# Optimization experiments

Hardware: AMD Instinct MI355X
Metric: run time of the kernel (lower is better)

Reference implementation:

```python
import jax, jax.numpy as jnp
import numpy as np

SEQ_LEN = 512
DIM = 256
HEADS = 8
DIM_HEAD = 32
INNER = HEADS * DIM_HEAD
BATCH = 1
LN_EPS = 1e-5


def setup_inputs() -> dict:
    key = jax.random.key(0)
    ks = jax.random.split(key, 6)
    # kaiming_uniform_(a=sqrt(5)) on [L, in, out] -> bound = 1/sqrt(fan_in) with fan_in = in_dim*out_dim? 
    # torch computes fan_in from dims [1:] => fan_in = in_dim (dim of -2) * ... in practice bound ~ sqrt(1/fan_in);
    # exact init distribution is irrelevant for correctness testing, use uniform(+-1/sqrt(DIM)).
    s = 1.0 / np.sqrt(DIM)
    so = 1.0 / np.sqrt(INNER)
    return {
        "x": jax.random.normal(ks[0], (BATCH, SEQ_LEN, DIM), jnp.float32),
        "Wq": jax.random.uniform(ks[1], (SEQ_LEN, DIM, INNER), jnp.float32, -s, s),
        "Wk": jax.random.uniform(ks[2], (SEQ_LEN, DIM, INNER), jnp.float32, -s, s),
        "Wv": jax.random.uniform(ks[3], (SEQ_LEN, DIM, INNER), jnp.float32, -s, s),
        "gamma": jnp.ones((DIM,), jnp.float32),
        "beta": jnp.zeros((DIM,), jnp.float32),
        "Wo": jax.random.uniform(ks[4], (INNER, DIM), jnp.float32, -so, so),
        "bo": jnp.zeros((DIM,), jnp.float32),
    }


def reference(x, Wq, Wk, Wv, gamma, beta, Wo, bo):
    b, n, dim = x.shape
    h, dh = HEADS, DIM_HEAD
    # LayerNorm
    mu = jnp.mean(x, axis=-1, keepdims=True)
    var = jnp.mean((x - mu) ** 2, axis=-1, keepdims=True)
    xn = (x - mu) / jnp.sqrt(var + LN_EPS) * gamma + beta
    # Per-relative-index projections: pd[b, r, m, e] = xn[b, m] @ W[r]
    qd = jnp.einsum('bmc,rce->brme', xn, Wq)
    kd = jnp.einsum('bmc,rce->brme', xn, Wk)
    vd = jnp.einsum('bmc,rce->brme', xn, Wv)
    i = jnp.arange(n)
    # to_q / to_v index map: max(0, i - j); to_k (after rearrange swap) uses min(0, m - n) + n - 1
    rq = jnp.maximum(0, i[:, None] - i[None, :])          # [n(query), m(key)]
    rk = jnp.minimum(0, i[None, :] - i[:, None]) + n - 1  # [n, m]
    # q[b,n,m,e] = qd[b, rq[n,m], m]; k[b,n,m,e] = kd[b, rk[n,m], n]; v like q
    q_full = qd[:, rq, i[None, :], :].reshape(b, n, n, h, dh)
    k_full = kd[:, rk, i[:, None], :].reshape(b, n, n, h, dh)
    v_full = vd[:, rq, i[None, :], :].reshape(b, n, n, h, dh)
    scale = dh ** -0.5
    dots = jnp.einsum('bnmhd,bnmhd->bhnm', q_full, k_full) * scale
    causal = i[:, None] >= i[None, :]  # tril
    dots = jnp.where(causal[None, None], dots, -jnp.inf)
    attn = jax.nn.softmax(dots, axis=-1)
    out = jnp.einsum('bhnm,bnmhd->bnhd', attn, v_full).reshape(b, n, h * dh)
    return out @ Wo + bo
```

## Files before the change

kernel.cpp:

```cpp
#include <hip/hip_runtime.h>
#include <hip/hip_bf16.h>

typedef unsigned short u16;
typedef unsigned int   u32;
typedef __bf16 bf16x8 __attribute__((ext_vector_type(8)));
typedef float  f32x4  __attribute__((ext_vector_type(4)));
typedef u32    u32x4  __attribute__((ext_vector_type(4)));
typedef u32    u32x2  __attribute__((ext_vector_type(2)));

#define TRI_TOTAL 131328

__device__ __forceinline__ float b2f(u16 u) {
    return __builtin_bit_cast(float, ((u32)u) << 16);
}
__device__ __forceinline__ u16 f2b(float f) {
    return __builtin_bit_cast(u16, __float2bfloat16(f));
}
__device__ __forceinline__ int pcol(int col) {
    return (((col & 7) ^ ((col >> 3) & 7)) << 4);
}
__device__ __forceinline__ void gload_lds16(const void* g, void* l) {
    __builtin_amdgcn_global_load_lds(
        (const __attribute__((address_space(1))) void*)g,
        (__attribute__((address_space(3))) void*)l, 16, 0, 0);
}

__global__ void __launch_bounds__(256) ln_kernel(const float* __restrict__ x,
                                                 const float* __restrict__ g,
                                                 const float* __restrict__ b,
                                                 u16* __restrict__ xn) {
    int n = blockIdx.x, t = threadIdx.x;
    float v = x[n * 256 + t];
    __shared__ float red[4];
    float s = v;
    #pragma unroll
    for (int o = 32; o >= 1; o >>= 1) s += __shfl_xor(s, o);
    if ((t & 63) == 0) red[t >> 6] = s;
    __syncthreads();
    float mu = (red[0] + red[1] + red[2] + red[3]) * (1.0f / 256.0f);
    float d = v - mu;
    __syncthreads();
    float s2 = d * d;
    #pragma unroll
    for (int o = 32; o >= 1; o >>= 1) s2 += __shfl_xor(s2, o);
    if ((t & 63) == 0) red[t >> 6] = s2;
    __syncthreads();
    float var = (red[0] + red[1] + red[2] + red[3]) * (1.0f / 256.0f);
    float y = d * rsqrtf(var + 1e-5f) * g[t] + b[t];
    xn[n * 256 + t] = f2b(y);
}

__global__ void __launch_bounds__(256) proj_kernel(
        const u16* __restrict__ xn,
        const float* __restrict__ Wq, const float* __restrict__ Wk,
        const float* __restrict__ Wv,
        u16* __restrict__ Qa, u16* __restrict__ Ka, u16* __restrict__ Va) {
    __shared__ char lds[65536];
    char* buf0 = lds;
    char* buf1 = lds + 32768;

    int bid = blockIdx.x;
    int which = bid >> 11;
    int rr = bid & 2047;
    int r  = (which == 1) ? (511 - (rr >> 2)) : (rr >> 2);
    int cs = rr & 3;
    const float* W = (which == 0) ? Wq : ((which == 1) ? Wk : Wv);
    u16* Out       = (which == 0) ? Qa : ((which == 1) ? Ka : Va);
    int rows  = (which == 1) ? (r + 1) : (512 - r);
    int pbase = (which == 1) ? (511 - r) : 0;
    int nbase = (which == 1) ? (511 - r) : r;

    int t = threadIdx.x;
    int c0 = cs * 64;
    int wv  = t >> 6;
    int rg  = wv >> 1;
    int cg  = wv & 1;
    int L   = t & 63;
    int l15 = L & 15, l4 = L >> 4;

#define DMA_TILE(DST, M0) do {                                                \
    _Pragma("unroll")                                                         \
    for (int j = 0; j < 8; ++j) {                                             \
        int lrow = wv * 16 + 2 * j + (L >> 5);                                \
        int grow = pbase + (M0) + lrow; if (grow > 511) grow = 511;           \
        const char* gp = (const char*)xn + (size_t)grow * 512                 \
                         + (((L & 31) ^ (lrow & 7)) << 4);                    \
        char* lp = (DST) + (wv * 16 + 2 * j) * 512;                           \
        gload_lds16(gp, lp);                                                  \
    }                                                                         \
} while (0)

    DMA_TILE(buf1, 0);

    {
        int c4 = (t & 15) * 4;
        int kq = t >> 4;
        const float* wp = W + ((size_t)r << 16) + c0 + c4 + (size_t)(kq * 4) * 256;
        f32x4 w00 = *(const f32x4*)(wp + 0);
        f32x4 w01 = *(const f32x4*)(wp + 256);
        f32x4 w02 = *(const f32x4*)(wp + 512);
        f32x4 w03 = *(const f32x4*)(wp + 768);
        f32x4 w10 = *(const f32x4*)(wp + 16384 + 0);
        f32x4 w11 = *(const f32x4*)(wp + 16384 + 256);
        f32x4 w12 = *(const f32x4*)(wp + 16384 + 512);
        f32x4 w13 = *(const f32x4*)(wp + 16384 + 768);
        f32x4 w20 = *(const f32x4*)(wp + 32768 + 0);
        f32x4 w21 = *(const f32x4*)(wp + 32768 + 256);
        f32x4 w22 = *(const f32x4*)(wp + 32768 + 512);
        f32x4 w23 = *(const f32x4*)(wp + 32768 + 768);
        f32x4 w30 = *(const f32x4*)(wp + 49152 + 0);
        f32x4 w31 = *(const f32x4*)(wp + 49152 + 256);
        f32x4 w32 = *(const f32x4*)(wp + 49152 + 512);
        f32x4 w33 = *(const f32x4*)(wp + 49152 + 768);
#define WLW(IT, VA, VB, VC, VD) {                                             \
        int kbase2 = (kq * 4 + (IT) * 64) * 2;                                \
        _Pragma("unroll")                                                     \
        for (int i = 0; i < 4; ++i) {                                         \
            int col = c4 + i;                                                 \
            u32 lo = (u32)f2b(VA[i]) | ((u32)f2b(VB[i]) << 16);               \
            u32 hi = (u32)f2b(VC[i]) | ((u32)f2b(VD[i]) << 16);               \
            u32x2 pr; pr[0] = lo; pr[1] = hi;                                 \
            *(u32x2*)(buf0 + col * 512 + (kbase2 ^ pcol(col))) = pr;          \
        }                                                                     \
    }
        WLW(0, w00, w01, w02, w03)
        WLW(1, w10, w11, w12, w13)
        WLW(2, w20, w21, w22, w23)
        WLW(3, w30, w31, w32, w33)
#undef WLW
    }
    __syncthreads();

    bf16x8 b00, b01, b02, b03, b04, b05, b06, b07;
    bf16x8 b10, b11, b12, b13, b14, b15, b16, b17;
#define BEXT(HF, KSI, DST) {                                                  \
    int col = cg * 32 + (HF) * 16 + l15;                                      \
    int kb = (KSI) * 64 + l4 * 16;                                            \
    DST = *(const bf16x8*)(buf0 + col * 512 + (kb ^ pcol(col))); }
    BEXT(0, 0, b00) BEXT(0, 1, b01) BEXT(0, 2, b02) BEXT(0, 3, b03)
    BEXT(0, 4, b04) BEXT(0, 5, b05) BEXT(0, 6, b06) BEXT(0, 7, b07)
    BEXT(1, 0, b10) BEXT(1, 1, b11) BEXT(1, 2, b12) BEXT(1, 3, b13)
    BEXT(1, 4, b14) BEXT(1, 5, b15) BEXT(1, 6, b16) BEXT(1, 7, b17)
#undef BEXT
    __syncthreads();

    int am = (l15 & 7) << 4;
    int nt = (rows + 63) >> 6;
    char* cur = buf1;
    char* alt = buf0;

    for (int i = 0; i < nt; ++i) {
        int m0 = i << 6;
        if (i + 1 < nt) DMA_TILE(alt, m0 + 64);

        const char* abase = cur + (rg * 32 + l15) * 512;
        f32x4 acc00 = {}, acc01 = {}, acc10 = {}, acc11 = {};
#define KS(ks) {                                                              \
        int kb = (ks) * 64 + l4 * 16;                                         \
        bf16x8 a0 = *(const bf16x8*)(abase + (kb ^ am));                      \
        bf16x8 a1 = *(const bf16x8*)(abase + 16 * 512 + (kb ^ am));           \
        acc00 = __builtin_amdgcn_mfma_f32_16x16x32_bf16(a0, b0##ks, acc00, 0, 0, 0); \
        acc01 = __builtin_amdgcn_mfma_f32_16x16x32_bf16(a0, b1##ks, acc01, 0, 0, 0); \
        acc10 = __builtin_amdgcn_mfma_f32_16x16x32_bf16(a1, b0##ks, acc10, 0, 0, 0); \
        acc11 = __builtin_amdgcn_mfma_f32_16x16x32_bf16(a1, b1##ks, acc11, 0, 0, 0); \
    }
        KS(0) KS(1) KS(2) KS(3) KS(4) KS(5) KS(6) KS(7)
#undef KS

        #pragma unroll
        for (int rf = 0; rf < 2; ++rf) {
            #pragma unroll
            for (int j = 0; j < 4; ++j) {
                int ml = m0 + rg * 32 + rf * 16 + l4 * 4 + j;
                if (ml < rows) {
                    u32 nout = (u32)(nbase + ml);
                    u32 prow = (nout * (nout + 1)) >> 1;
                    u16* op = Out + (size_t)((u32)(prow + (u32)ml)) * 256
                              + c0 + cg * 32 + l15;
                    f32x4 va = rf ? acc10 : acc00;
                    f32x4 vb = rf ? acc11 : acc01;
                    op[0]  = f2b(va[j]);
                    op[16] = f2b(vb[j]);
                }
            }
        }
        asm volatile("s_waitcnt vmcnt(16)" ::: "memory");
        __builtin_amdgcn_s_barrier();
        __builtin_amdgcn_sched_barrier(0);
        char* tmp = cur; cur = alt; alt = tmp;
    }
#undef DMA_TILE
}

__global__ void __launch_bounds__(256) attn_kernel(const u16* __restrict__ Qa,
                                                   const u16* __restrict__ Ka,
                                                   const u16* __restrict__ Va,
                                                   float* __restrict__ ao) {
    int n = 511 - blockIdx.x, t = threadIdx.x;
    __shared__ float pbuf[512 * 9];
    __shared__ float linv[8];
    int band = n + 1;
    size_t rb = (size_t)(n * (n + 1) / 2);

    int h = t & 7, mi = t >> 3;
    for (int m0 = 0; m0 < band; m0 += 32) {
        int m = m0 + mi;
        float d = -1e30f;
        if (m < band) {
            const char* qp = (const char*)Qa + (rb + m) * 512 + h * 64;
            const char* kp = (const char*)Ka + (rb + m) * 512 + h * 64;
            float acc = 0.f;
            #pragma unroll
            for (int cch = 0; cch < 4; ++cch) {
                u32x4 qv = *reinterpret_cast<const u32x4*>(qp + cch * 16);
                u32x4 kv = *reinterpret_cast<const u32x4*>(kp + cch * 16);
                #pragma unroll
                for (int i = 0; i < 4; ++i) {
                    float ql = __builtin_bit_cast(float, qv[i] << 16);
                    float qh = __builtin_bit_cast(float, qv[i] & 0xffff0000u);
                    float kl = __builtin_bit_cast(float, kv[i] << 16);
                    float kh = __builtin_bit_cast(float, kv[i] & 0xffff0000u);
                    acc += ql * kl + qh * kh;
                }
            }
            d = acc * 0.17677669529663687f;
        }
        pbuf[m * 9 + h] = d;
    }
    __syncthreads();

    int wv = t >> 6, L = t & 63;
    for (int s = 0; s < 2; ++s) {
        int hh = wv + s * 4;
        float mx = -1e30f;
        for (int m = L; m < band; m += 64) mx = fmaxf(mx, pbuf[m * 9 + hh]);
        #pragma unroll
        for (int o = 32; o >= 1; o >>= 1) mx = fmaxf(mx, __shfl_xor(mx, o));
        float sum = 0.f;
        for (int m = L; m < band; m += 64) {
            float p = __expf(pbuf[m * 9 + hh] - mx);
            pbuf[m * 9 + hh] = p;
            sum += p;
        }
        #pragma unroll
        for (int o = 32; o >= 1; o >>= 1) sum += __shfl_xor(sum, o);
        if (L == 0) linv[hh] = 1.0f / sum;
    }
    __syncthreads();

    int h2 = t >> 5;
    const char* vp = (const char*)Va + rb * 512 + (size_t)t * 2;
    const float* pb = pbuf + h2;
    float a0 = 0, a1 = 0, a2 = 0, a3 = 0, a4 = 0, a5 = 0, a6 = 0, a7 = 0;
    int m = 0;
    for (; m + 16 <= band; m += 16) {
        u16 v0  = *(const u16*)(vp + (size_t)(m +  0) * 512);
        u16 v1  = *(const u16*)(vp + (size_t)(m +  1) * 512);
        u16 v2  = *(const u16*)(vp + (size_t)(m +  2) * 512);
        u16 v3  = *(const u16*)(vp + (size_t)(m +  3) * 512);
        u16 v4  = *(const u16*)(vp + (size_t)(m +  4) * 512);
        u16 v5  = *(const u16*)(vp + (size_t)(m +  5) * 512);
        u16 v6  = *(const u16*)(vp + (size_t)(m +  6) * 512);
        u16 v7  = *(const u16*)(vp + (size_t)(m +  7) * 512);
        u16 v8  = *(const u16*)(vp + (size_t)(m +  8) * 512);
        u16 v9  = *(const u16*)(vp + (size_t)(m +  9) * 512);
        u16 v10 = *(const u16*)(vp + (size_t)(m + 10) * 512);
        u16 v11 = *(const u16*)(vp + (size_t)(m + 11) * 512);
        u16 v12 = *(const u16*)(vp + (size_t)(m + 12) * 512);
        u16 v13 = *(const u16*)(vp + (size_t)(m + 13) * 512);
        u16 v14 = *(const u16*)(vp + (size_t)(m + 14) * 512);
        u16 v15 = *(const u16*)(vp + (size_t)(m + 15) * 512);
        a0 += pb[(m +  0) * 9] * b2f(v0);
        a1 += pb[(m +  1) * 9] * b2f(v1);
        a2 += pb[(m +  2) * 9] * b2f(v2);
        a3 += pb[(m +  3) * 9] * b2f(v3);
        a4 += pb[(m +  4) * 9] * b2f(v4);
        a5 += pb[(m +  5) * 9] * b2f(v5);
        a6 += pb[(m +  6) * 9] * b2f(v6);
        a7 += pb[(m +  7) * 9] * b2f(v7);
        a0 += pb[(m +  8) * 9] * b2f(v8);
        a1 += pb[(m +  9) * 9] * b2f(v9);
        a2 += pb[(m + 10) * 9] * b2f(v10);
        a3 += pb[(m + 11) * 9] * b2f(v11);
        a4 += pb[(m + 12) * 9] * b2f(v12);
        a5 += pb[(m + 13) * 9] * b2f(v13);
        a6 += pb[(m + 14) * 9] * b2f(v14);
        a7 += pb[(m + 15) * 9] * b2f(v15);
    }
    for (; m < band; ++m)
        a0 += pb[m * 9] * b2f(*(const u16*)(vp + (size_t)m * 512));
    ao[n * 256 + t] = (((a0 + a1) + (a2 + a3)) + ((a4 + a5) + (a6 + a7)))
                      * linv[h2];
}

__global__ void __launch_bounds__(256) outproj_kernel(const float* __restrict__ ao,
                                                      const float* __restrict__ Wo,
                                                      const float* __restrict__ bo,
                                                      float* __restrict__ out) {
    int n = blockIdx.x, e = threadIdx.x;
    const float* a = ao + n * 256;
    float c0 = bo[e], c1 = 0, c2 = 0, c3 = 0;
    for (int c = 0; c < 256; c += 4) {
        c0 += a[c + 0] * Wo[(c + 0) * 256 + e];
        c1 += a[c + 1] * Wo[(c + 1) * 256 + e];
        c2 += a[c + 2] * Wo[(c + 2) * 256 + e];
        c3 += a[c + 3] * Wo[(c + 3) * 256 + e];
    }
    out[n * 256 + e] = (c0 + c1) + (c2 + c3);
}

extern "C" void kernel_launch(void* const* d_in, const int* in_sizes, int n_in,
                              void* d_out, int out_size, void* d_ws, size_t ws_size,
                              hipStream_t stream) {
    const float* x     = (const float*)d_in[0];
    const float* Wq    = (const float*)d_in[1];
    const float* Wk    = (const float*)d_in[2];
    const float* Wv    = (const float*)d_in[3];
    const float* gamma = (const float*)d_in[4];
    const float* beta  = (const float*)d_in[5];
    const float* Wo    = (const float*)d_in[6];
    const float* bo    = (const float*)d_in[7];
    float* out = (float*)d_out;

    char* ws = (char*)d_ws;
    u16* xn = (u16*)ws;
    size_t off = (size_t)512 * 256 * 2;
    u16* Qa = (u16*)(ws + off); off += (size_t)TRI_TOTAL * 256 * 2;
    u16* Ka = (u16*)(ws + off); off += (size_t)TRI_TOTAL * 256 * 2;
    u16* Va = (u16*)(ws + off); off += (size_t)TRI_TOTAL * 256 * 2;
    float* ao = (float*)(ws + off);

    ln_kernel<<<512, 256, 0, stream>>>(x, gamma, beta, xn);
    proj_kernel<<<6144, 256, 0, stream>>>(xn, Wq, Wk, Wv, Qa, Ka, Va);
    attn_kernel<<<512, 256, 0, stream>>>(Qa, Ka, Va, ao);
    outproj_kernel<<<512, 256, 0, stream>>>(ao, Wo, bo, out);
}
```

Measured before the change: 236.9 us.

## Process four relative indices per projection block and prefetch next weights via DMA

Each proj_kernel block now handles four consecutive relative indices r instead of one, so the grid drops from 6144 to 1536 blocks. Blocks are interleaved by Q/K/V with bid%3. During the last activation tile of one r, half of the next r's fp32 weight slab is prefetched into LDS with global_load_lds, and the other half comes from direct global loads. The weights are then converted to swizzled bf16 in place. The aim is to hide weight-load latency and cut per-block startup cost, at the price of fewer blocks for load balancing and extra barriers and LDS round-trips between r values.

```diff
diff --git a/kernel.cpp b/kernel.cpp
--- a/kernel.cpp
+++ b/kernel.cpp
@@ -56,19 +56,16 @@
         const float* __restrict__ Wv,
         u16* __restrict__ Qa, u16* __restrict__ Ka, u16* __restrict__ Va) {
     __shared__ char lds[65536];
-    char* buf0 = lds;
-    char* buf1 = lds + 32768;
+    char* bufA = lds;
+    char* bufB = lds + 32768;
 
     int bid = blockIdx.x;
-    int which = bid >> 11;
-    int rr = bid & 2047;
-    int r  = (which == 1) ? (511 - (rr >> 2)) : (rr >> 2);
+    int which = bid % 3;
+    int rr = bid / 3;
+    int strip = rr >> 2;
     int cs = rr & 3;
     const float* W = (which == 0) ? Wq : ((which == 1) ? Wk : Wv);
     u16* Out       = (which == 0) ? Qa : ((which == 1) ? Ka : Va);
-    int rows  = (which == 1) ? (r + 1) : (512 - r);
-    int pbase = (which == 1) ? (511 - r) : 0;
-    int nbase = (which == 1) ? (511 - r) : r;
 
     int t = threadIdx.x;
     int c0 = cs * 64;
@@ -77,6 +74,18 @@
     int cg  = wv & 1;
     int L   = t & 63;
     int l15 = L & 15, l4 = L >> 4;
+    int c4 = (t & 15) * 4;
+    int kq = t >> 4;
+
+    int r, rows, pbase, nbase;
+#define SET_R(Q) do {                                                         \
+    int rq_ = strip * 4 + (Q);                                                \
+    r = (which == 1) ? (511 - rq_) : rq_;                                     \
+    rows  = (which == 1) ? (r + 1) : (512 - r);                               \
+    pbase = (which == 1) ? (511 - r) : 0;                                     \
+    nbase = (which == 1) ? (511 - r) : r;                                     \
+} while (0)
+    SET_R(0);
 
 #define DMA_TILE(DST, M0) do {                                                \
     _Pragma("unroll")                                                         \
@@ -90,11 +99,32 @@
     }                                                                         \
 } while (0)
 
-    DMA_TILE(buf1, 0);
+#define DMA_WHALF(DST, R) do {                                                \
+    const char* wsrc = (const char*)(W + ((size_t)(R) << 16) + c0);           \
+    _Pragma("unroll")                                                         \
+    for (int p = 0; p < 8; ++p) {                                             \
+        int kk = p * 16 + (t >> 4);                                           \
+        const char* gp = wsrc + (size_t)kk * 1024 + (t & 15) * 16;            \
+        char* lp = (DST) + p * 4096 + (t >> 6) * 1024;                        \
+        gload_lds16(gp, lp);                                                  \
+    }                                                                         \
+} while (0)
+
+#define WLW(DST, IT, VA, VB, VC, VD) {                                        \
+        int kbase2 = (kq * 4 + (IT) * 64) * 2;                                \
+        _Pragma("unroll")                                                     \
+        for (int i = 0; i < 4; ++i) {                                         \
+            int col = c4 + i;                                                 \
+            u32 lo = (u32)f2b(VA[i]) | ((u32)f2b(VB[i]) << 16);               \
+            u32 hi = (u32)f2b(VC[i]) | ((u32)f2b(VD[i]) << 16);               \
+            u32x2 pr; pr[0] = lo; pr[1] = hi;                                 \
+            *(u32x2*)((DST) + col * 512 + (kbase2 ^ pcol(col))) = pr;         \
+        }                                                                     \
+    }
+
+    DMA_TILE(bufB, 0);
 
     {
-        int c4 = (t & 15) * 4;
-        int kq = t >> 4;
         const float* wp = W + ((size_t)r << 16) + c0 + c4 + (size_t)(kq * 4) * 256;
         f32x4 w00 = *(const f32x4*)(wp + 0);
         f32x4 w01 = *(const f32x4*)(wp + 256);
@@ -112,49 +142,57 @@
         f32x4 w31 = *(const f32x4*)(wp + 49152 + 256);
         f32x4 w32 = *(const f32x4*)(wp + 49152 + 512);
         f32x4 w33 = *(const f32x4*)(wp + 49152 + 768);
-#define WLW(IT, VA, VB, VC, VD) {                                             \
-        int kbase2 = (kq * 4 + (IT) * 64) * 2;                                \
-        _Pragma("unroll")                                                     \
-        for (int i = 0; i < 4; ++i) {                                         \
-            int col = c4 + i;                                                 \
-            u32 lo = (u32)f2b(VA[i]) | ((u32)f2b(VB[i]) << 16);               \
-            u32 hi = (u32)f2b(VC[i]) | ((u32)f2b(VD[i]) << 16);               \
-            u32x2 pr; pr[0] = lo; pr[1] = hi;                                 \
-            *(u32x2*)(buf0 + col * 512 + (kbase2 ^ pcol(col))) = pr;          \
-        }                                                                     \
-    }
-        WLW(0, w00, w01, w02, w03)
-        WLW(1, w10, w11, w12, w13)
-        WLW(2, w20, w21, w22, w23)
-        WLW(3, w30, w31, w32, w33)
-#undef WLW
+        WLW(bufA, 0, w00, w01, w02, w03)
+        WLW(bufA, 1, w10, w11, w12, w13)
+        WLW(bufA, 2, w20, w21, w22, w23)
+        WLW(bufA, 3, w30, w31, w32, w33)
     }
     __syncthreads();
 
     bf16x8 b00, b01, b02, b03, b04, b05, b06, b07;
     bf16x8 b10, b11, b12, b13, b14, b15, b16, b17;
-#define BEXT(HF, KSI, DST) {                                                  \
-    int col = cg * 32 + (HF) * 16 + l15;                                      \
-    int kb = (KSI) * 64 + l4 * 16;                                            \
-    DST = *(const bf16x8*)(buf0 + col * 512 + (kb ^ pcol(col))); }
-    BEXT(0, 0, b00) BEXT(0, 1, b01) BEXT(0, 2, b02) BEXT(0, 3, b03)
-    BEXT(0, 4, b04) BEXT(0, 5, b05) BEXT(0, 6, b06) BEXT(0, 7, b07)
-    BEXT(1, 0, b10) BEXT(1, 1, b11) BEXT(1, 2, b12) BEXT(1, 3, b13)
-    BEXT(1, 4, b14) BEXT(1, 5, b15) BEXT(1, 6, b16) BEXT(1, 7, b17)
-#undef BEXT
+#define BEXT(SRC) do {                                                        \
+    int colA_ = cg * 32 + l15, colB_ = cg * 32 + 16 + l15;                    \
+    _Pragma("unroll")                                                         \
+    for (int dummy = 0; dummy < 1; ++dummy) {                                 \
+        b00 = *(const bf16x8*)((SRC) + colA_ * 512 + ((0*64 + l4*16) ^ pcol(colA_))); \
+        b01 = *(const bf16x8*)((SRC) + colA_ * 512 + ((1*64 + l4*16) ^ pcol(colA_))); \
+        b02 = *(const bf16x8*)((SRC) + colA_ * 512 + ((2*64 + l4*16) ^ pcol(colA_))); \
+        b03 = *(const bf16x8*)((SRC) + colA_ * 512 + ((3*64 + l4*16) ^ pcol(colA_))); \
+        b04 = *(const bf16x8*)((SRC) + colA_ * 512 + ((4*64 + l4*16) ^ pcol(colA_))); \
+        b05 = *(const bf16x8*)((SRC) + colA_ * 512 + ((5*64 + l4*16) ^ pcol(colA_))); \
+        b06 = *(const bf16x8*)((SRC) + colA_ * 512 + ((6*64 + l4*16) ^ pcol(colA_))); \
+        b07 = *(const bf16x8*)((SRC) + colA_ * 512 + ((7*64 + l4*16) ^ pcol(colA_))); \
+        b10 = *(const bf16x8*)((SRC) + colB_ * 512 + ((0*64 + l4*16) ^ pcol(colB_))); \
+        b11 = *(const bf16x8*)((SRC) + colB_ * 512 + ((1*64 + l4*16) ^ pcol(colB_))); \
+        b12 = *(const bf16x8*)((SRC) + colB_ * 512 + ((2*64 + l4*16) ^ pcol(colB_))); \
+        b13 = *(const bf16x8*)((SRC) + colB_ * 512 + ((3*64 + l4*16) ^ pcol(colB_))); \
+        b14 = *(const bf16x8*)((SRC) + colB_ * 512 + ((4*64 + l4*16) ^ pcol(colB_))); \
+        b15 = *(const bf16x8*)((SRC) + colB_ * 512 + ((5*64 + l4*16) ^ pcol(colB_))); \
+        b16 = *(const bf16x8*)((SRC) + colB_ * 512 + ((6*64 + l4*16) ^ pcol(colB_))); \
+        b17 = *(const bf16x8*)((SRC) + colB_ * 512 + ((7*64 + l4*16) ^ pcol(colB_))); \
+    }                                                                         \
+} while (0)
+    BEXT(bufA);
     __syncthreads();
 
     int am = (l15 & 7) << 4;
-    int nt = (rows + 63) >> 6;
-    char* cur = buf1;
-    char* alt = buf0;
-
-    for (int i = 0; i < nt; ++i) {
-        int m0 = i << 6;
-        if (i + 1 < nt) DMA_TILE(alt, m0 + 64);
-
-        const char* abase = cur + (rg * 32 + l15) * 512;
-        f32x4 acc00 = {}, acc01 = {}, acc10 = {}, acc11 = {};
+    char* cur = bufB;
+    char* alt = bufA;
+
+    for (int q = 0;;) {
+        int rnext = 0;
+        if (q < 3) { int rq_ = strip * 4 + q + 1;
+                     rnext = (which == 1) ? (511 - rq_) : rq_; }
+        int nt = (rows + 63) >> 6;
+        for (int i = 0; i < nt; ++i) {
+            int m0 = i << 6;
+            bool lastt = (i + 1 >= nt);
+            if (!lastt)          DMA_TILE(alt, m0 + 64);
+            else if (q < 3)      DMA_WHALF(alt, rnext);
+
+            const char* abase = cur + (rg * 32 + l15) * 512;
+            f32x4 acc00 = {}, acc01 = {}, acc10 = {}, acc11 = {};
 #define KS(ks) {                                                              \
         int kb = (ks) * 64 + l4 * 16;                                         \
         bf16x8 a0 = *(const bf16x8*)(abase + (kb ^ am));                      \
@@ -164,32 +202,67 @@
         acc10 = __builtin_amdgcn_mfma_f32_16x16x32_bf16(a1, b0##ks, acc10, 0, 0, 0); \
         acc11 = __builtin_amdgcn_mfma_f32_16x16x32_bf16(a1, b1##ks, acc11, 0, 0, 0); \
     }
-        KS(0) KS(1) KS(2) KS(3) KS(4) KS(5) KS(6) KS(7)
+            KS(0) KS(1) KS(2) KS(3) KS(4) KS(5) KS(6) KS(7)
 #undef KS
-
-        #pragma unroll
-        for (int rf = 0; rf < 2; ++rf) {
             #pragma unroll
-            for (int j = 0; j < 4; ++j) {
-                int ml = m0 + rg * 32 + rf * 16 + l4 * 4 + j;
-                if (ml < rows) {
-                    u32 nout = (u32)(nbase + ml);
-                    u32 prow = (nout * (nout + 1)) >> 1;
-                    u16* op = Out + (size_t)((u32)(prow + (u32)ml)) * 256
-                              + c0 + cg * 32 + l15;
-                    f32x4 va = rf ? acc10 : acc00;
-                    f32x4 vb = rf ? acc11 : acc01;
-                    op[0]  = f2b(va[j]);
-                    op[16] = f2b(vb[j]);
+            for (int rf = 0; rf < 2; ++rf) {
+                #pragma unroll
+                for (int j = 0; j < 4; ++j) {
+                    int ml = m0 + rg * 32 + rf * 16 + l4 * 4 + j;
+                    if (ml < rows) {
+                        u32 nout = (u32)(nbase + ml);
+                        u32 prow = (nout * (nout + 1)) >> 1;
+                        u16* op = Out + (size_t)(prow + (u32)ml) * 256
+                                  + c0 + cg * 32 + l15;
+                        f32x4 va = rf ? acc10 : acc00;
+                        f32x4 vb = rf ? acc11 : acc01;
+                        op[0]  = f2b(va[j]);
+                        op[16] = f2b(vb[j]);
+                    }
                 }
             }
+            if (!lastt) { asm volatile("s_waitcnt vmcnt(16)" ::: "memory"); }
+            else        { asm volatile("s_waitcnt vmcnt(0)"  ::: "memory"); }
+            __builtin_amdgcn_s_barrier();
+            __builtin_amdgcn_sched_barrier(0);
+            { char* tmp = cur; cur = alt; alt = tmp; }
         }
-        asm volatile("s_waitcnt vmcnt(16)" ::: "memory");
-        __builtin_amdgcn_s_barrier();
-        __builtin_amdgcn_sched_barrier(0);
-        char* tmp = cur; cur = alt; alt = tmp;
+        if (++q > 3) break;
+        SET_R(q);
+        DMA_TILE(alt, 0);
+        const float* wpg = W + ((size_t)r << 16) + c0 + c4;
+        f32x4 gw0 = *(const f32x4*)(wpg + 32768 + (size_t)(kq * 4 + 0) * 256);
+        f32x4 gw1 = *(const f32x4*)(wpg + 32768 + (size_t)(kq * 4 + 1) * 256);
+        f32x4 gw2 = *(const f32x4*)(wpg + 32768 + (size_t)(kq * 4 + 2) * 256);
+        f32x4 gw3 = *(const f32x4*)(wpg + 32768 + (size_t)(kq * 4 + 3) * 256);
+        f32x4 gw4 = *(const f32x4*)(wpg + 49152 + (size_t)(kq * 4 + 0) * 256);
+        f32x4 gw5 = *(const f32x4*)(wpg + 49152 + (size_t)(kq * 4 + 1) * 256);
+        f32x4 gw6 = *(const f32x4*)(wpg + 49152 + (size_t)(kq * 4 + 2) * 256);
+        f32x4 gw7 = *(const f32x4*)(wpg + 49152 + (size_t)(kq * 4 + 3) * 256);
+        f32x4 lw0 = *(const f32x4*)(cur + (kq * 4 + 0) * 256 + (t & 15) * 16);
+        f32x4 lw1 = *(const f32x4*)(cur + (kq * 4 + 1) * 256 + (t & 15) * 16);
+        f32x4 lw2 = *(const f32x4*)(cur + (kq * 4 + 2) * 256 + (t & 15) * 16);
+        f32x4 lw3 = *(const f32x4*)(cur + (kq * 4 + 3) * 256 + (t & 15) * 16);
+        f32x4 lw4 = *(const f32x4*)(cur + (64 + kq * 4 + 0) * 256 + (t & 15) * 16);
+        f32x4 lw5 = *(const f32x4*)(cur + (64 + kq * 4 + 1) * 256 + (t & 15) * 16);
+        f32x4 lw6 = *(const f32x4*)(cur + (64 + kq * 4 + 2) * 256 + (t & 15) * 16);
+        f32x4 lw7 = *(const f32x4*)(cur + (64 + kq * 4 + 3) * 256 + (t & 15) * 16);
+        __syncthreads();
+        WLW(cur, 0, lw0, lw1, lw2, lw3)
+        WLW(cur, 1, lw4, lw5, lw6, lw7)
+        WLW(cur, 2, gw0, gw1, gw2, gw3)
+        WLW(cur, 3, gw4, gw5, gw6, gw7)
+        asm volatile("s_waitcnt vmcnt(0)" ::: "memory");
+        __syncthreads();
+        BEXT(cur);
+        __syncthreads();
+        { char* tmp = cur; cur = alt; alt = tmp; }
     }
 #undef DMA_TILE
+#undef DMA_WHALF
+#undef WLW
+#undef BEXT
+#undef SET_R
 }
 
 __global__ void __launch_bounds__(256) attn_kernel(const u16* __restrict__ Qa,
@@ -331,7 +404,7 @@
     float* ao = (float*)(ws + off);
 
     ln_kernel<<<512, 256, 0, stream>>>(x, gamma, beta, xn);
-    proj_kernel<<<6144, 256, 0, stream>>>(xn, Wq, Wk, Wv, Qa, Ka, Va);
+    proj_kernel<<<1536, 256, 0, stream>>>(xn, Wq, Wk, Wv, Qa, Ka, Va);
     attn_kernel<<<512, 256, 0, stream>>>(Qa, Ka, Va, ao);
     outproj_kernel<<<512, 256, 0, stream>>>(ao, Wo, bo, out);
 }
```

New measurement: 234.2 us. Within noise of the previous version (-1.1%).
